# Performance work log

Measured on AMD Instinct MI355X. Metric: run time of the kernel, lower is better.

The kernel has to match this reference:

```python
import jax, jax.numpy as jnp
import numpy as np

V = 778   # MANO mesh vertex count (hard-coded in the module)
K = 9     # spiral neighborhood length
C = 256   # in_channels
OUT = 3   # out_channels (per-vertex offset xyz)
B3 = 192  # 3 * B, B = 64


def setup_inputs() -> dict:
    key = jax.random.key(0)
    ks = jax.random.split(key, 12)
    x = jax.random.normal(ks[0], (B3, V, C), jnp.float32)
    pred_occ = jax.random.normal(ks[1], (B3, 2, 5), jnp.float32)
    indices = jax.random.randint(ks[2], (V, K), 0, V)
    finger_sizes = [112, 120, 124, 116, 108]
    fingers = {f"finger{i}": jax.random.randint(ks[3 + i], (n,), 0, V)
               for i, n in enumerate(finger_sizes)}

    def lin(k, fan_in, fan_out):
        kw, kb = jax.random.split(k)
        w = jax.random.normal(kw, (fan_in, fan_out), jnp.float32) / np.float32(np.sqrt(fan_in))
        b = jax.random.normal(kb, (fan_out,), jnp.float32) * 0.01
        return w, b

    w0, b0 = lin(ks[8], 2 * C * K, 2 * C)
    w1, b1 = lin(ks[9], 2 * C * K, C)
    w2, b2 = lin(ks[10], C * K, C)
    wh, bh = lin(ks[11], C * K, OUT)
    return {"x": x, "pred_occ": pred_occ, "indices": indices, **fingers,
            "w0": w0, "b0": b0, "w1": w1, "b1": b1, "w2": w2, "b2": b2,
            "wh": wh, "bh": bh}


def spiral_conv(x, idx, w, b):
    # x: [B, V, Cin], idx: [V, K] -> gather spiral neighbors, flatten, linear
    B = x.shape[0]
    g = x[:, idx.reshape(-1), :].reshape(B, V, -1)  # [B, V, K*Cin]
    return g @ w + b


def reference(x, pred_occ, indices, finger0, finger1, finger2, finger3, finger4,
              w0, b0, w1, b1, w2, b2, wh, bh):
    # Per-finger non-occlusion probabilities: softmax over class dim, take class 0
    occ = jax.nn.softmax(pred_occ, axis=1)[:, 0, :5]          # [3B, 5]
    weights = jnp.ones((x.shape[0], V), x.dtype)
    for i, fidx in enumerate([finger0, finger1, finger2, finger3, finger4]):
        val = jnp.broadcast_to(occ[:, i:i + 1], (x.shape[0], fidx.shape[0]))
        weights = weights.at[:, fidx].set(val)
    B = x.shape[0] // 3
    wv = jnp.stack(jnp.split(weights, 3, axis=0), axis=-1)[..., None]  # [B, V, 3, 1]
    wv = jax.nn.softmax(wv, axis=2)
    xv = jnp.stack(jnp.split(x, 3, axis=0), axis=2)                    # [B, V, 3, C]
    wx = jnp.sum(wv * xv, axis=2)                                      # [B, V, C]
    h = jnp.concatenate([wx, x[:B]], axis=2)                           # [B, V, 2C]
    h = jax.nn.relu(spiral_conv(h, indices, w0, b0))
    h = jax.nn.relu(spiral_conv(h, indices, w1, b1))
    h = jax.nn.relu(spiral_conv(h, indices, w2, b2))
    return spiral_conv(h, indices, wh, bh)                             # [B, V, 3]
```

## Files before the change

kernel.cpp:

```cpp
#include <hip/hip_runtime.h>

typedef unsigned short ushort_t;
typedef __attribute__((ext_vector_type(8))) __bf16 bf16x8;
typedef __attribute__((ext_vector_type(8))) unsigned short ushort8;
typedef __attribute__((ext_vector_type(4))) float floatx4;
typedef __attribute__((ext_vector_type(16))) float floatx16;

#define VN 778
#define KNB 9

__device__ __forceinline__ float bf2f(unsigned short s) {
  union { unsigned int u; float f; } x; x.u = ((unsigned int)s) << 16; return x.f;
}
__device__ __forceinline__ unsigned short f2bf(float f) {
  union { float f; unsigned int u; } x; x.f = f;
  unsigned int r = x.u + 0x7fffu + ((x.u >> 16) & 1u);
  return (unsigned short)(r >> 16);
}

__device__ __forceinline__ void load_lds16(const void* g, void* l) {
  __builtin_amdgcn_global_load_lds(
      (const __attribute__((address_space(1))) unsigned int*)g,
      (__attribute__((address_space(3))) unsigned int*)l, 16, 0, 0);
}

__global__ void prep_misc(const float* __restrict__ pred_occ,
                          const int* f0, const int* f1, const int* f2,
                          const int* f3, const int* f4,
                          int n0, int n1, int n2, int n3, int n4,
                          const float* __restrict__ wh,
                          float* __restrict__ occ, int* __restrict__ fid,
                          float* __restrict__ whT) {
  int t = threadIdx.x;
  for (int i = t; i < 192 * 5; i += 256) {
    int r = i / 5, f = i % 5;
    float p0 = pred_occ[r * 10 + f];
    float p1 = pred_occ[r * 10 + 5 + f];
    occ[i] = 1.0f / (1.0f + __expf(p1 - p0));
  }
  for (int i = t; i < VN; i += 256) fid[i] = -1;
  __syncthreads();
  const int* fp[5] = {f0, f1, f2, f3, f4};
  int fn[5] = {n0, n1, n2, n3, n4};
  for (int fi = 0; fi < 5; ++fi) {
    for (int i = t; i < fn[fi]; i += 256) fid[fp[fi][i]] = fi;
    __syncthreads();
  }
  for (int i = t; i < 3 * 2304; i += 256) {
    int o = i / 2304, k = i % 2304;
    whT[i] = wh[k * 3 + o];
  }
}

__global__ void wx_kernel(const float* __restrict__ x, const float* __restrict__ occ,
                          const int* __restrict__ fid, ushort_t* __restrict__ wx) {
  int g = blockIdx.x * 256 + threadIdx.x;
  int c8 = (g & 31) << 3;
  int bv = g >> 5;
  int b = bv / VN;
  int v = bv - b * VN;
  int f = fid[v];
  float w0 = 1.f, w1 = 1.f, w2 = 1.f;
  if (f >= 0) {
    w0 = occ[b * 5 + f];
    w1 = occ[(64 + b) * 5 + f];
    w2 = occ[(128 + b) * 5 + f];
  }
  float m = fmaxf(w0, fmaxf(w1, w2));
  float e0 = __expf(w0 - m), e1 = __expf(w1 - m), e2 = __expf(w2 - m);
  float inv = 1.0f / (e0 + e1 + e2);
  e0 *= inv; e1 *= inv; e2 *= inv;
  size_t base = (size_t)bv * 256 + c8;
  const size_t V1 = (size_t)64 * VN * 256, V2 = (size_t)128 * VN * 256;
  floatx4 x0a = *(const floatx4*)(x + base);
  floatx4 x0b = *(const floatx4*)(x + base + 4);
  floatx4 x1a = *(const floatx4*)(x + V1 + base);
  floatx4 x1b = *(const floatx4*)(x + V1 + base + 4);
  floatx4 x2a = *(const floatx4*)(x + V2 + base);
  floatx4 x2b = *(const floatx4*)(x + V2 + base + 4);
  ushort8 o;
#pragma unroll
  for (int e = 0; e < 4; ++e) {
    o[e]     = f2bf(e0 * x0a[e] + e1 * x1a[e] + e2 * x2a[e]);
    o[e + 4] = f2bf(e0 * x0b[e] + e1 * x1b[e] + e2 * x2b[e]);
  }
  *(ushort8*)(wx + base) = o;
}

__global__ void xcvt_kernel(const float* __restrict__ x, ushort_t* __restrict__ xb) {
  int g = blockIdx.x * 256 + threadIdx.x;
  size_t base = (size_t)g * 8;
  floatx4 fa = *(const floatx4*)(x + base);
  floatx4 fb = *(const floatx4*)(x + base + 4);
  ushort8 o;
#pragma unroll
  for (int e = 0; e < 4; ++e) { o[e] = f2bf(fa[e]); o[e + 4] = f2bf(fb[e]); }
  *(ushort8*)(xb + base) = o;
}

__global__ void pack_w(const float* __restrict__ w, ushort_t* __restrict__ wP,
                       int N, int ksn, int total) {
  int chunk = blockIdx.x * 256 + threadIdx.x;
  if (chunk >= total) return;
  int lane = chunk & 63;
  int rest = chunk >> 6;
  int ks = rest % ksn;
  int tn = rest / ksn;
  int n = (tn << 5) + (lane & 31);
  int kb = (ks << 4) + ((lane >> 5) << 3);
  ushort8 o;
#pragma unroll
  for (int j = 0; j < 8; ++j) o[j] = f2bf(w[(size_t)(kb + j) * N + n]);
  *(ushort8*)(wP + (size_t)chunk * 8) = o;
}

template <int CIN, int MODE>
__global__ __launch_bounds__(256, 4) void spiral_g(
    const ushort_t* __restrict__ act0, const float* __restrict__ actF,
    const ushort_t* __restrict__ actB, const ushort_t* __restrict__ wP,
    const float* __restrict__ bias, const int* __restrict__ idx,
    ushort_t* __restrict__ out, int NOUT) {
  constexpr int H = CIN / 128;
  constexpr int P = KNB * H;
  __shared__ __align__(16) ushort_t Alds[2][1024 * 8];
  const int v = blockIdx.x;
  const int n0 = blockIdx.y << 8;
  const int tid = threadIdx.x;
  const int lane = tid & 63;
  const int wv = tid >> 6;
  const int mlo = lane & 31;
  const int q = lane >> 5;
  floatx16 acc00{}, acc01{}, acc10{}, acc11{};
  const int KtotSteps = KNB * (CIN / 16);
  const int tn0 = (n0 >> 5) + (wv << 1);
  const ushort_t* bp0 = wP + (size_t)tn0 * KtotSteps * 512 + lane * 8;
  const ushort_t* bp1 = bp0 + (size_t)KtotSteps * 512;
  const int* iv = idx + v * KNB;
  const int xm = mlo & 7;

  auto dma_stage = [&](int p, ushort_t* buf) {
    const int nbr = p / H, h = p - nbr * H;
    const int nv = iv[nbr];
#pragma unroll
    for (int it = 0; it < 4; ++it) {
      const int S = (wv << 2) + it;
      const int row = (S << 2) + (lane >> 4);
      const int ck = (lane & 15) ^ (row & 7);
      const ushort_t* src;
      if (MODE == 0)
        src = act0 + ((size_t)(row * VN + nv)) * CIN + h * 128 + ck * 8;
      else if (MODE == 2 && h >= 2)
        src = actB + ((size_t)(row * VN + nv)) * 256 + (h - 2) * 128 + ck * 8;
      else
        src = act0 + ((size_t)(row * VN + nv)) * 256 + h * 128 + ck * 8;
      load_lds16(src, buf + (size_t)S * 512);
    }
  };
  auto f32_stage = [&](int p, ushort_t* buf) {
    const int nbr = p / H, h = p - nbr * H;
    const int nv = iv[nbr];
#pragma unroll
    for (int j = 0; j < 4; ++j) {
      const int c = (j << 8) + tid;
      const int row = c >> 4;
      const int ck = (c & 15) ^ (row & 7);
      const float* src = actF + ((size_t)(row * VN + nv)) * 256 + (h - 2) * 128 + ck * 8;
      floatx4 fa = *(const floatx4*)src;
      floatx4 fb = *(const floatx4*)(src + 4);
      ushort8 o;
#pragma unroll
      for (int e = 0; e < 4; ++e) { o[e] = f2bf(fa[e]); o[e + 4] = f2bf(fb[e]); }
      *(ushort8*)(buf + (size_t)c * 8) = o;
    }
  };

  dma_stage(0, Alds[0]);
  __syncthreads();
#pragma unroll 2
  for (int p = 0; p < P; ++p) {
    ushort_t* cur = Alds[p & 1];
    ushort_t* nxt = Alds[(p + 1) & 1];
    const bool have_next = (p + 1 < P);
    const bool next_f32 = (MODE == 1) && (((p + 1) & (H - 1)) >= 2);
    if (have_next && !next_f32) dma_stage(p + 1, nxt);
#pragma unroll
    for (int ks = 0; ks < 8; ++ks) {
      const int cko = ((ks << 1) + q) ^ xm;
      const int ch0 = (mlo << 4) + cko;
      bf16x8 a0 = *(const bf16x8*)(cur + (size_t)ch0 * 8);
      bf16x8 a1 = *(const bf16x8*)(cur + (size_t)(ch0 + 512) * 8);
      bf16x8 b0v = *(const bf16x8*)bp0; bp0 += 512;
      bf16x8 b1v = *(const bf16x8*)bp1; bp1 += 512;
      acc00 = __builtin_amdgcn_mfma_f32_32x32x16_bf16(a0, b0v, acc00, 0, 0, 0);
      acc10 = __builtin_amdgcn_mfma_f32_32x32x16_bf16(a1, b0v, acc10, 0, 0, 0);
      acc01 = __builtin_amdgcn_mfma_f32_32x32x16_bf16(a0, b1v, acc01, 0, 0, 0);
      acc11 = __builtin_amdgcn_mfma_f32_32x32x16_bf16(a1, b1v, acc11, 0, 0, 0);
    }
    __syncthreads();
    if (have_next && next_f32) { f32_stage(p + 1, nxt); __syncthreads(); }
  }
  const int na = n0 + (wv << 6) + mlo;
  const int nb = na + 32;
  const float bna = bias[na];
  const float bnb = bias[nb];
#pragma unroll
  for (int t = 0; t < 4; ++t) {
    const floatx16 av = (t == 0) ? acc00 : (t == 1) ? acc10 : (t == 2) ? acc01 : acc11;
    const int bbase = (t & 1) << 5;
    const int n = (t < 2) ? na : nb;
    const float bn = (t < 2) ? bna : bnb;
#pragma unroll
    for (int r = 0; r < 16; ++r) {
      const int m = (r & 3) + ((r >> 2) << 3) + (q << 2);
      float val = av[r] + bn; val = val > 0.f ? val : 0.f;
      out[((size_t)((bbase + m) * VN + v)) * NOUT + n] = f2bf(val);
    }
  }
}

__global__ void head_kernel(const ushort_t* __restrict__ act, const float* __restrict__ whT,
                            const float* __restrict__ bh, const int* __restrict__ idx,
                            float* __restrict__ out) {
  __shared__ __align__(16) ushort_t Alds[64 * 256];
  const int v = blockIdx.x;
  const int tid = threadIdx.x;
  float a0 = 0.f, a1 = 0.f, a2 = 0.f;
  const int b = tid;
  const int xm = b & 7;
  for (int nbr = 0; nbr < KNB; ++nbr) {
    const int nv = idx[v * KNB + nbr];
    __syncthreads();
#pragma unroll
    for (int it = 0; it < 8; ++it) {
      int L = it * 256 + tid;
      int bb = L >> 5;
      int jj = L & 31;
      ushort8 val = *(const ushort8*)(act + ((size_t)(bb * VN + nv)) * 256 + (jj << 3));
      int slot = jj ^ (bb & 7);
      *(ushort8*)&Alds[(size_t)(bb * 32 + slot) * 8] = val;
    }
    __syncthreads();
    if (tid < 64) {
      const float* wp = whT + nbr * 256;
#pragma unroll 4
      for (int j = 0; j < 32; ++j) {
        int jj = j ^ xm;
        ushort8 a8 = *(const ushort8*)&Alds[(b * 32 + jj) * 8];
#pragma unroll
        for (int e = 0; e < 8; ++e) {
          float av = bf2f(a8[e]);
          int k = (j << 3) + e;
          a0 += av * wp[k];
          a1 += av * wp[2304 + k];
          a2 += av * wp[4608 + k];
        }
      }
    }
  }
  if (tid < 64) {
    size_t o = ((size_t)(b * VN + v)) * 3;
    out[o + 0] = a0 + bh[0];
    out[o + 1] = a1 + bh[1];
    out[o + 2] = a2 + bh[2];
  }
}

extern "C" void kernel_launch(void* const* d_in, const int* in_sizes, int n_in,
                              void* d_out, int out_size, void* d_ws, size_t ws_size,
                              hipStream_t stream) {
  const float* x        = (const float*)d_in[0];
  const float* pred_occ = (const float*)d_in[1];
  const int* indices    = (const int*)d_in[2];
  const int* f0 = (const int*)d_in[3];
  const int* f1 = (const int*)d_in[4];
  const int* f2 = (const int*)d_in[5];
  const int* f3 = (const int*)d_in[6];
  const int* f4 = (const int*)d_in[7];
  const float* w0 = (const float*)d_in[8];
  const float* b0 = (const float*)d_in[9];
  const float* w1 = (const float*)d_in[10];
  const float* b1 = (const float*)d_in[11];
  const float* w2 = (const float*)d_in[12];
  const float* b2 = (const float*)d_in[13];
  const float* wh = (const float*)d_in[14];
  const float* bh = (const float*)d_in[15];
  float* outp = (float*)d_out;

  char* ws = (char*)d_ws;
  ushort_t* wP0 = (ushort_t*)(ws + 0);
  ushort_t* wP1 = (ushort_t*)(ws + 4718592);
  ushort_t* wP2 = (ushort_t*)(ws + 7077888);
  float* whT    = (float*)(ws + 8257536);
  float* occ    = (float*)(ws + 8285184);
  int* fid      = (int*)(ws + 8289024);
  ushort_t* R0  = (ushort_t*)(ws + 8292352);
  ushort_t* R1  = (ushort_t*)(ws + 33785856);
  ushort_t* XB  = (ushort_t*)(ws + 84772864);
  const bool useXB = (ws_size >= 110266368ull);

  prep_misc<<<1, 256, 0, stream>>>(pred_occ, f0, f1, f2, f3, f4,
                                   in_sizes[3], in_sizes[4], in_sizes[5],
                                   in_sizes[6], in_sizes[7], wh, occ, fid, whT);
  pack_w<<<294912 / 256, 256, 0, stream>>>(w0, wP0, 512, 288, 294912);
  pack_w<<<147456 / 256, 256, 0, stream>>>(w1, wP1, 256, 288, 147456);
  pack_w<<<73728 / 256, 256, 0, stream>>>(w2, wP2, 256, 144, 73728);
  if (useXB) xcvt_kernel<<<6224, 256, 0, stream>>>(x, XB);
  wx_kernel<<<6224, 256, 0, stream>>>(x, occ, fid, R0);

  if (useXB)
    spiral_g<512, 2><<<dim3(VN, 2), 256, 0, stream>>>(R0, nullptr, XB, wP0, b0,
                                                      indices, R1, 512);
  else
    spiral_g<512, 1><<<dim3(VN, 2), 256, 0, stream>>>(R0, x, nullptr, wP0, b0,
                                                      indices, R1, 512);
  spiral_g<512, 0><<<dim3(VN, 1), 256, 0, stream>>>(R1, nullptr, nullptr, wP1, b1,
                                                    indices, R0, 256);
  spiral_g<256, 0><<<dim3(VN, 1), 256, 0, stream>>>(R0, nullptr, nullptr, wP2, b2,
                                                    indices, R1, 256);
  head_kernel<<<VN, 256, 0, stream>>>(R1, whT, bh, indices, outp);
  (void)n_in; (void)out_size;
}
```

Baseline: 940.9 us.

## Replace LDS DMA staging with register-prefetched loads overlapping MFMA compute

The spiral conv kernel now prefetches the next neighbor tile into registers before the MFMA loop and writes it to LDS afterward, replacing global_load_lds DMA and the separate synchronous f32 staging pass. The f32 half of the first layer input is converted inline from registers, which removes the xcvt pre-conversion kernel and the extra bf16 copy of x. Launch bounds drop from 4 to 3 blocks per SM to make room for the extra prefetch registers. The aim is to hide gather latency behind compute and remove an extra barrier and kernel, at the cost of higher register pressure and lower occupancy.

```diff
diff --git a/kernel.cpp b/kernel.cpp
--- a/kernel.cpp
+++ b/kernel.cpp
@@ -16,12 +16,6 @@
   union { float f; unsigned int u; } x; x.f = f;
   unsigned int r = x.u + 0x7fffu + ((x.u >> 16) & 1u);
   return (unsigned short)(r >> 16);
-}
-
-__device__ __forceinline__ void load_lds16(const void* g, void* l) {
-  __builtin_amdgcn_global_load_lds(
-      (const __attribute__((address_space(1))) unsigned int*)g,
-      (__attribute__((address_space(3))) unsigned int*)l, 16, 0, 0);
 }
 
 __global__ void prep_misc(const float* __restrict__ pred_occ,
@@ -87,17 +81,6 @@
   *(ushort8*)(wx + base) = o;
 }
 
-__global__ void xcvt_kernel(const float* __restrict__ x, ushort_t* __restrict__ xb) {
-  int g = blockIdx.x * 256 + threadIdx.x;
-  size_t base = (size_t)g * 8;
-  floatx4 fa = *(const floatx4*)(x + base);
-  floatx4 fb = *(const floatx4*)(x + base + 4);
-  ushort8 o;
-#pragma unroll
-  for (int e = 0; e < 4; ++e) { o[e] = f2bf(fa[e]); o[e + 4] = f2bf(fb[e]); }
-  *(ushort8*)(xb + base) = o;
-}
-
 __global__ void pack_w(const float* __restrict__ w, ushort_t* __restrict__ wP,
                        int N, int ksn, int total) {
   int chunk = blockIdx.x * 256 + threadIdx.x;
@@ -115,11 +98,10 @@
 }
 
 template <int CIN, int MODE>
-__global__ __launch_bounds__(256, 4) void spiral_g(
+__global__ __launch_bounds__(256, 3) void spiral_g(
     const ushort_t* __restrict__ act0, const float* __restrict__ actF,
-    const ushort_t* __restrict__ actB, const ushort_t* __restrict__ wP,
-    const float* __restrict__ bias, const int* __restrict__ idx,
-    ushort_t* __restrict__ out, int NOUT) {
+    const ushort_t* __restrict__ wP, const float* __restrict__ bias,
+    const int* __restrict__ idx, ushort_t* __restrict__ out, int NOUT) {
   constexpr int H = CIN / 128;
   constexpr int P = KNB * H;
   __shared__ __align__(16) ushort_t Alds[2][1024 * 8];
@@ -130,63 +112,65 @@
   const int wv = tid >> 6;
   const int mlo = lane & 31;
   const int q = lane >> 5;
+  const int xm = mlo & 7;
   floatx16 acc00{}, acc01{}, acc10{}, acc11{};
   const int KtotSteps = KNB * (CIN / 16);
   const int tn0 = (n0 >> 5) + (wv << 1);
   const ushort_t* bp0 = wP + (size_t)tn0 * KtotSteps * 512 + lane * 8;
   const ushort_t* bp1 = bp0 + (size_t)KtotSteps * 512;
   const int* iv = idx + v * KNB;
-  const int xm = mlo & 7;
-
-  auto dma_stage = [&](int p, ushort_t* buf) {
-    const int nbr = p / H, h = p - nbr * H;
-    const int nv = iv[nbr];
-#pragma unroll
-    for (int it = 0; it < 4; ++it) {
-      const int S = (wv << 2) + it;
-      const int row = (S << 2) + (lane >> 4);
-      const int ck = (lane & 15) ^ (row & 7);
-      const ushort_t* src;
-      if (MODE == 0)
-        src = act0 + ((size_t)(row * VN + nv)) * CIN + h * 128 + ck * 8;
-      else if (MODE == 2 && h >= 2)
-        src = actB + ((size_t)(row * VN + nv)) * 256 + (h - 2) * 128 + ck * 8;
-      else
-        src = act0 + ((size_t)(row * VN + nv)) * 256 + h * 128 + ck * 8;
-      load_lds16(src, buf + (size_t)S * 512);
-    }
-  };
-  auto f32_stage = [&](int p, ushort_t* buf) {
-    const int nbr = p / H, h = p - nbr * H;
-    const int nv = iv[nbr];
+  const int srow = tid >> 4;
+  const int ck8 = (((tid & 15) ^ (srow & 7)) << 3);
+  ushort8 sreg[4];
+
+  {
+    const int nv = iv[0];
+    const int rs = (MODE == 1) ? 256 : CIN;
 #pragma unroll
     for (int j = 0; j < 4; ++j) {
-      const int c = (j << 8) + tid;
-      const int row = c >> 4;
-      const int ck = (c & 15) ^ (row & 7);
-      const float* src = actF + ((size_t)(row * VN + nv)) * 256 + (h - 2) * 128 + ck * 8;
-      floatx4 fa = *(const floatx4*)src;
-      floatx4 fb = *(const floatx4*)(src + 4);
-      ushort8 o;
-#pragma unroll
-      for (int e = 0; e < 4; ++e) { o[e] = f2bf(fa[e]); o[e + 4] = f2bf(fb[e]); }
-      *(ushort8*)(buf + (size_t)c * 8) = o;
-    }
-  };
-
-  dma_stage(0, Alds[0]);
+      const int row = (j << 4) + srow;
+      sreg[j] = *(const ushort8*)(act0 + ((size_t)(row * VN + nv)) * rs + ck8);
+    }
+#pragma unroll
+    for (int j = 0; j < 4; ++j)
+      *(ushort8*)&Alds[0][(size_t)((j << 8) + tid) * 8] = sreg[j];
+  }
   __syncthreads();
+
 #pragma unroll 2
   for (int p = 0; p < P; ++p) {
-    ushort_t* cur = Alds[p & 1];
-    ushort_t* nxt = Alds[(p + 1) & 1];
+    const ushort_t* cur = Alds[p & 1];
+    ushort_t* nxt = (ushort_t*)Alds[(p + 1) & 1];
     const bool have_next = (p + 1 < P);
-    const bool next_f32 = (MODE == 1) && (((p + 1) & (H - 1)) >= 2);
-    if (have_next && !next_f32) dma_stage(p + 1, nxt);
+    bool nf32 = false;
+    floatx4 freg[8];
+    if (have_next) {
+      const int pn = p + 1;
+      const int nbr = pn / H, h = pn - nbr * H;
+      const int nv = iv[nbr];
+      if (MODE == 1 && h >= 2) {
+        nf32 = true;
+#pragma unroll
+        for (int j = 0; j < 4; ++j) {
+          const int row = (j << 4) + srow;
+          const float* src = actF + ((size_t)(row * VN + nv)) * 256 + (h - 2) * 128 + ck8;
+          freg[2 * j]     = *(const floatx4*)src;
+          freg[2 * j + 1] = *(const floatx4*)(src + 4);
+        }
+      } else {
+#pragma unroll
+        for (int j = 0; j < 4; ++j) {
+          const int row = (j << 4) + srow;
+          const ushort_t* src;
+          if (MODE == 0) src = act0 + ((size_t)(row * VN + nv)) * CIN + h * 128 + ck8;
+          else           src = act0 + ((size_t)(row * VN + nv)) * 256 + h * 128 + ck8;
+          sreg[j] = *(const ushort8*)src;
+        }
+      }
+    }
 #pragma unroll
     for (int ks = 0; ks < 8; ++ks) {
-      const int cko = ((ks << 1) + q) ^ xm;
-      const int ch0 = (mlo << 4) + cko;
+      const int ch0 = (mlo << 4) + (((ks << 1) + q) ^ xm);
       bf16x8 a0 = *(const bf16x8*)(cur + (size_t)ch0 * 8);
       bf16x8 a1 = *(const bf16x8*)(cur + (size_t)(ch0 + 512) * 8);
       bf16x8 b0v = *(const bf16x8*)bp0; bp0 += 512;
@@ -196,8 +180,25 @@
       acc01 = __builtin_amdgcn_mfma_f32_32x32x16_bf16(a0, b1v, acc01, 0, 0, 0);
       acc11 = __builtin_amdgcn_mfma_f32_32x32x16_bf16(a1, b1v, acc11, 0, 0, 0);
     }
+    if (have_next) {
+      if (nf32) {
+#pragma unroll
+        for (int j = 0; j < 4; ++j) {
+          ushort8 o;
+#pragma unroll
+          for (int e = 0; e < 4; ++e) {
+            o[e]     = f2bf(freg[2 * j][e]);
+            o[e + 4] = f2bf(freg[2 * j + 1][e]);
+          }
+          *(ushort8*)&nxt[(size_t)((j << 8) + tid) * 8] = o;
+        }
+      } else {
+#pragma unroll
+        for (int j = 0; j < 4; ++j)
+          *(ushort8*)&nxt[(size_t)((j << 8) + tid) * 8] = sreg[j];
+      }
+    }
     __syncthreads();
-    if (have_next && next_f32) { f32_stage(p + 1, nxt); __syncthreads(); }
   }
   const int na = n0 + (wv << 6) + mlo;
   const int nb = na + 32;
@@ -295,8 +296,6 @@
   int* fid      = (int*)(ws + 8289024);
   ushort_t* R0  = (ushort_t*)(ws + 8292352);
   ushort_t* R1  = (ushort_t*)(ws + 33785856);
-  ushort_t* XB  = (ushort_t*)(ws + 84772864);
-  const bool useXB = (ws_size >= 110266368ull);
 
   prep_misc<<<1, 256, 0, stream>>>(pred_occ, f0, f1, f2, f3, f4,
                                    in_sizes[3], in_sizes[4], in_sizes[5],
@@ -304,19 +303,11 @@
   pack_w<<<294912 / 256, 256, 0, stream>>>(w0, wP0, 512, 288, 294912);
   pack_w<<<147456 / 256, 256, 0, stream>>>(w1, wP1, 256, 288, 147456);
   pack_w<<<73728 / 256, 256, 0, stream>>>(w2, wP2, 256, 144, 73728);
-  if (useXB) xcvt_kernel<<<6224, 256, 0, stream>>>(x, XB);
   wx_kernel<<<6224, 256, 0, stream>>>(x, occ, fid, R0);
 
-  if (useXB)
-    spiral_g<512, 2><<<dim3(VN, 2), 256, 0, stream>>>(R0, nullptr, XB, wP0, b0,
-                                                      indices, R1, 512);
-  else
-    spiral_g<512, 1><<<dim3(VN, 2), 256, 0, stream>>>(R0, x, nullptr, wP0, b0,
-                                                      indices, R1, 512);
-  spiral_g<512, 0><<<dim3(VN, 1), 256, 0, stream>>>(R1, nullptr, nullptr, wP1, b1,
-                                                    indices, R0, 256);
-  spiral_g<256, 0><<<dim3(VN, 1), 256, 0, stream>>>(R0, nullptr, nullptr, wP2, b2,
-                                                    indices, R1, 256);
+  spiral_g<512, 1><<<dim3(VN, 2), 256, 0, stream>>>(R0, x, wP0, b0, indices, R1, 512);
+  spiral_g<512, 0><<<dim3(VN, 1), 256, 0, stream>>>(R1, nullptr, wP1, b1, indices, R0, 256);
+  spiral_g<256, 0><<<dim3(VN, 1), 256, 0, stream>>>(R0, nullptr, wP2, b2, indices, R1, 256);
   head_kernel<<<VN, 256, 0, stream>>>(R1, whT, bh, indices, outp);
-  (void)n_in; (void)out_size;
-}
+  (void)n_in; (void)out_size; (void)ws_size;
+}
```

New measurement: 2.359 ms. 151% more time.
